# Kernel optimization log

Hardware: AMD Instinct MI355X
Metric: run time of the kernel (lower is better)

## Reference

```python
import jax, jax.numpy as jnp
import numpy as np

BN_EPS = 1e-5


def _fps(xyz, n_centers):
    """Furthest point sampling. xyz: (B,N,3) -> idx (B,n_centers) int32.
    Deterministic start at index 0 (torch version uses randint start)."""
    B, N, _ = xyz.shape
    batch_ar = jnp.arange(B)

    def step(carry, _):
        distances, farthest = carry  # (B,N), (B,)
        center = xyz[batch_ar, farthest]  # (B,3)
        d = jnp.sum((xyz - center[:, None, :]) ** 2, axis=-1)  # (B,N)
        distances = jnp.minimum(distances, d)
        new_far = jnp.argmax(distances, axis=-1)
        return (distances, new_far), farthest

    init = (jnp.full((B, N), jnp.inf, dtype=xyz.dtype),
            jnp.zeros((B,), dtype=jnp.int32))
    _, idxs = jax.lax.scan(step, init, None, length=n_centers)  # (n_centers, B)
    return idxs.T  # (B, n_centers)


def _knn_group(xyz, centers, k):
    """xyz:(B,N,3), centers:(B,M,3) -> patches (B,M,k,3) center-relative."""
    # (B,M,N) squared distances
    dists = jnp.sum((centers[:, :, None, :] - xyz[:, None, :, :]) ** 2, axis=-1)
    _, idx = jax.lax.top_k(-dists, k)  # (B,M,k) smallest distances
    # gather neighbor coords: (B,M,k,3)
    patches = jnp.take_along_axis(xyz[:, None, :, :], idx[..., None], axis=2)
    return patches - centers[:, :, None, :]


def _bn_eval(x, gamma, beta):
    # BatchNorm1d in eval mode: running_mean=0, running_var=1
    return x * (gamma / jnp.sqrt(1.0 + BN_EPS)) + beta


def _mini_pointnet(patches, W1, b1, g1, bt1, W2, b2, g2, bt2, W3, b3, g3, bt3):
    B, M, k, C = patches.shape
    x = patches.reshape(B * M * k, C)
    x = jax.nn.relu(_bn_eval(x @ W1 + b1, g1, bt1))
    x = jax.nn.relu(_bn_eval(x @ W2 + b2, g2, bt2))
    x = jax.nn.relu(_bn_eval(x @ W3 + b3, g3, bt3))
    x = x.reshape(B * M, k, -1).max(axis=1)
    return x.reshape(B, M, -1)


def setup_inputs() -> dict:
    key = jax.random.key(0)
    ks = jax.random.split(key, 8)
    B, N = 16, 16384
    embed = 256

    def lin(kk, fan_in, fan_out):
        bound = 1.0 / np.sqrt(fan_in)
        k1, k2 = jax.random.split(kk)
        W = jax.random.uniform(k1, (fan_in, fan_out), jnp.float32, -bound, bound)
        b = jax.random.uniform(k2, (fan_out,), jnp.float32, -bound, bound)
        return W, b

    W1, b1 = lin(ks[1], 3, 64)
    W2, b2 = lin(ks[2], 64, 128)
    W3, b3 = lin(ks[3], 128, embed)
    return {
        "xyz": jax.random.normal(ks[0], (B, N, 3), jnp.float32),
        "W1": W1, "b1": b1, "g1": jnp.ones((64,)), "bt1": jnp.zeros((64,)),
        "W2": W2, "b2": b2, "g2": jnp.ones((128,)), "bt2": jnp.zeros((128,)),
        "W3": W3, "b3": b3, "g3": jnp.ones((embed,)), "bt3": jnp.zeros((embed,)),
        "n_centers": 256,
        "k": 32,
    }


def reference(xyz, W1, b1, g1, bt1, W2, b2, g2, bt2, W3, b3, g3, bt3,
              n_centers, k):
    center_idx = _fps(xyz, n_centers)  # (B, M)
    centers = jnp.take_along_axis(xyz, center_idx[..., None], axis=1)  # (B,M,3)
    patches = _knn_group(xyz, centers, k)  # (B,M,k,3)
    tokens = _mini_pointnet(patches, W1, b1, g1, bt1, W2, b2, g2, bt2,
                            W3, b3, g3, bt3)
    return tokens, centers
```

## Files before the change

### kernel.cpp

```cpp
#include <hip/hip_runtime.h>

constexpr int B   = 16;
constexpr int N   = 16384;
constexpr int M   = 256;
constexpr int K   = 32;
constexpr int EMB = 256;

__device__ __forceinline__ float sqdist(float px, float py, float pz,
                                        float cx, float cy, float cz) {
  float dx = __fsub_rn(px, cx);
  float dy = __fsub_rn(py, cy);
  float dz = __fsub_rn(pz, cz);
  return __fadd_rn(__fadd_rn(__fmul_rn(dx, dx), __fmul_rn(dy, dy)),
                   __fmul_rn(dz, dz));
}

constexpr int FT = 1024;
constexpr int FW = FT / 64;

__global__ __launch_bounds__(FT) void fps_kernel(
    const float* __restrict__ xyz, float* __restrict__ centers) {
  const int b = blockIdx.x;
  const int tid = threadIdx.x;
  const int lane = tid & 63;
  const int wid = tid >> 6;
  const int l15 = lane & 15;
  const float* base = xyz + (size_t)b * N * 3;
  const float4* b4 = (const float4*)base;

  __shared__ float4 s_d[4][FT];
  __shared__ float s_pv[2][FW];
  __shared__ int s_pn[2][FW];
  __shared__ int s_flag[FW];

  const float inf = __builtin_inff();
#pragma unroll
  for (int c = 0; c < 4; ++c) s_d[c][tid] = make_float4(inf, inf, inf, inf);
  if (tid < FW) s_flag[tid] = 0;

  float cx = base[0], cy = base[1], cz = base[2];
  __syncthreads();

  const int f0 = tid * 12;

  for (int it = 0; it < M; ++it) {
    if (tid == 0) {
      float* co = centers + ((size_t)b * M + it) * 3;
      co[0] = cx; co[1] = cy; co[2] = cz;
    }
    const int p = it & 1;

    float bv = -1.0f;
    int bj = 0;

#define FPS_UPD(D, J, X, Y, Z) {                           \
    float dx = __fsub_rn((X), cx);                         \
    float dy = __fsub_rn((Y), cy);                         \
    float dz = __fsub_rn((Z), cz);                         \
    float dd = __fadd_rn(__fadd_rn(__fmul_rn(dx, dx),      \
                                   __fmul_rn(dy, dy)),     \
                         __fmul_rn(dz, dz));               \
    float nd = fminf(D, dd);                               \
    D = nd;                                                \
    bool g = nd > bv;                                      \
    bv = g ? nd : bv;                                      \
    bj = g ? (J) : bj; }

#pragma unroll
    for (int c = 0; c < 4; ++c) {
      float4 qa = b4[f0 + c * 3 + 0];
      float4 qb = b4[f0 + c * 3 + 1];
      float4 qc = b4[f0 + c * 3 + 2];
      float4 dq = s_d[c][tid];
      FPS_UPD(dq.x, c * 4 + 0, qa.x, qa.y, qa.z)
      FPS_UPD(dq.y, c * 4 + 1, qa.w, qb.x, qb.y)
      FPS_UPD(dq.z, c * 4 + 2, qb.z, qb.w, qc.x)
      FPS_UPD(dq.w, c * 4 + 3, qc.y, qc.z, qc.w)
      s_d[c][tid] = dq;
    }
#undef FPS_UPD

    int bn = (tid << 4) + bj;

#pragma unroll
    for (int mm = 32; mm >= 1; mm >>= 1) {
      float ov = __shfl_xor(bv, mm, 64);
      int on = __shfl_xor(bn, mm, 64);
      if (ov > bv || (ov == bv && on < bn)) { bv = ov; bn = on; }
    }

    if (lane == 0) {
      s_pv[p][wid] = bv;
      s_pn[p][wid] = bn;
      asm volatile("s_waitcnt lgkmcnt(0)" ::: "memory");
      s_flag[wid] = it + 1;
    }

    {
      volatile int* vf = s_flag;
      while (!__all(vf[l15] >= it + 1)) {}
    }
    asm volatile("" ::: "memory");

    float v = s_pv[p][l15];
    int n = s_pn[p][l15];
#pragma unroll
    for (int mm = 1; mm <= 8; mm <<= 1) {
      float ov = __shfl_xor(v, mm, 16);
      int on = __shfl_xor(n, mm, 16);
      if (ov > v || (ov == v && on < n)) { v = ov; n = on; }
    }
    cx = base[(size_t)n * 3 + 0];
    cy = base[(size_t)n * 3 + 1];
    cz = base[(size_t)n * 3 + 2];
  }
}

constexpr int KT = 256;
constexpr int CAP = 512;
constexpr int NBUCKET = 1024;

__global__ __launch_bounds__(KT) void knn_kernel(
    const float* __restrict__ xyz, const float* __restrict__ centers,
    float* __restrict__ patches) {
  const int blk = blockIdx.x;
  const int b = blk >> 8;
  const int tid = threadIdx.x;
  const float* base = xyz + (size_t)b * N * 3;

  __shared__ int hist[NBUCKET];
  __shared__ unsigned cb[CAP];
  __shared__ int ci[CAP];
  __shared__ int s_nin, s_ncand, s_tb;
  __shared__ int s_wsum[KT / 64];
  __shared__ float s_cc[3];

  if (tid == 0) {
    const float* c = centers + (size_t)blk * 3;
    s_cc[0] = c[0]; s_cc[1] = c[1]; s_cc[2] = c[2];
    s_nin = 0; s_ncand = 0;
  }
  for (int i = tid; i < NBUCKET; i += KT) hist[i] = 0;
  __syncthreads();

  const float cx = s_cc[0], cy = s_cc[1], cz = s_cc[2];

  for (int n = tid; n < N; n += KT) {
    float d = sqdist(base[n * 3], base[n * 3 + 1], base[n * 3 + 2], cx, cy, cz);
    atomicAdd(&hist[__float_as_uint(d) >> 21], 1);
  }
  __syncthreads();

  int h0[4];
  int loc = 0;
#pragma unroll
  for (int i = 0; i < 4; ++i) { h0[i] = hist[tid * 4 + i]; loc += h0[i]; }
  int lane = tid & 63, wid = tid >> 6;
  int scan = loc;
  for (int off = 1; off < 64; off <<= 1) {
    int o = __shfl_up(scan, off, 64);
    if (lane >= off) scan += o;
  }
  if (lane == 63) s_wsum[wid] = scan;
  __syncthreads();
  int woff = 0;
  for (int w = 0; w < wid; ++w) woff += s_wsum[w];
  int c0 = woff + scan - loc;
#pragma unroll
  for (int i = 0; i < 4; ++i) {
    int c1 = c0 + h0[i];
    if (c0 < K && c1 >= K) s_tb = tid * 4 + i;
    c0 = c1;
  }
  __syncthreads();
  const int tb = s_tb;
  const unsigned lo = (unsigned)tb << 21;
  const unsigned hi = (unsigned)(tb + 1) << 21;

  for (int n = tid; n < N; n += KT) {
    float x = base[n * 3], y = base[n * 3 + 1], z = base[n * 3 + 2];
    float d = sqdist(x, y, z, cx, cy, cz);
    unsigned bits = __float_as_uint(d);
    if (bits < lo) {
      int pos = atomicAdd(&s_nin, 1);
      float* p = patches + ((size_t)blk * K + pos) * 3;
      p[0] = __fsub_rn(x, cx); p[1] = __fsub_rn(y, cy); p[2] = __fsub_rn(z, cz);
    } else if (bits < hi) {
      int q = atomicAdd(&s_ncand, 1);
      if (q < CAP) { cb[q] = bits; ci[q] = n; }
    }
  }
  __syncthreads();

  const int nin = s_nin;
  const int ncand = min(s_ncand, CAP);
  const int nsel = K - nin;
  for (int j = tid; j < ncand; j += KT) {
    unsigned bj = cb[j];
    int ij = ci[j];
    int rank = 0;
    for (int i2 = 0; i2 < ncand; ++i2) {
      unsigned bv = cb[i2];
      int iv = ci[i2];
      rank += (bv < bj || (bv == bj && iv < ij)) ? 1 : 0;
    }
    if (rank < nsel) {
      float x = base[ij * 3], y = base[ij * 3 + 1], z = base[ij * 3 + 2];
      float* p = patches + ((size_t)blk * K + nin + rank) * 3;
      p[0] = __fsub_rn(x, cx); p[1] = __fsub_rn(y, cy); p[2] = __fsub_rn(z, cz);
    }
  }
}

constexpr int MT = 128;

__global__ __launch_bounds__(MT) void mlp_kernel(
    const float* __restrict__ patches,
    const float* __restrict__ W1, const float* __restrict__ b1,
    const float* __restrict__ g1, const float* __restrict__ bt1,
    const float* __restrict__ W2, const float* __restrict__ b2,
    const float* __restrict__ g2, const float* __restrict__ bt2,
    const float* __restrict__ W3, const float* __restrict__ b3,
    const float* __restrict__ g3, const float* __restrict__ bt3,
    float* __restrict__ tokens) {
  const int pm = blockIdx.x;
  const int tid = threadIdx.x;
  __shared__ float xs[3][K];
  __shared__ float h1s[64 * K];
  __shared__ float h2s[128 * K];
  __shared__ float pms[2][EMB];

  const float* patch = patches + (size_t)pm * (K * 3);
  if (tid < 96) xs[tid % 3][tid / 3] = patch[tid];
  __syncthreads();

  const int cg = tid & 63;
  const int half = tid >> 6;
  const int pt0 = half * 16;
  const float rs = 1.0f / sqrtf(1.0f + 1e-5f);

  {
    const int c = cg;
    const float w0 = W1[c], w1 = W1[64 + c], w2 = W1[128 + c];
    const float bb = b1[c];
    const float sc = g1[c] * rs, be = bt1[c];
    float o[16];
#pragma unroll
    for (int p = 0; p < 16; ++p) {
      int pt = pt0 + p;
      float a = xs[0][pt] * w0 + xs[1][pt] * w1 + xs[2][pt] * w2 + bb;
      o[p] = fmaxf(a * sc + be, 0.0f);
    }
    const int so = (c & 7) << 2;
#pragma unroll
    for (int p4 = 0; p4 < 16; p4 += 4) {
      *(float4*)&h1s[c * K + ((pt0 + p4) ^ so)] =
          make_float4(o[p4], o[p4 + 1], o[p4 + 2], o[p4 + 3]);
    }
  }
  __syncthreads();

  {
    const int c = cg * 2;
    float acc0[16], acc1[16];
    const float bb0 = b2[c], bb1 = b2[c + 1];
#pragma unroll
    for (int p = 0; p < 16; ++p) { acc0[p] = bb0; acc1[p] = bb1; }
    for (int k = 0; k < 64; ++k) {
      const float2 w = *(const float2*)(W2 + k * 128 + c);
      const int so = (k & 7) << 2;
      float4 x0 = *(const float4*)&h1s[k * K + ((pt0 + 0) ^ so)];
      float4 x1 = *(const float4*)&h1s[k * K + ((pt0 + 4) ^ so)];
      float4 x2 = *(const float4*)&h1s[k * K + ((pt0 + 8) ^ so)];
      float4 x3 = *(const float4*)&h1s[k * K + ((pt0 + 12) ^ so)];
      float xv[16] = {x0.x, x0.y, x0.z, x0.w, x1.x, x1.y, x1.z, x1.w,
                      x2.x, x2.y, x2.z, x2.w, x3.x, x3.y, x3.z, x3.w};
#pragma unroll
      for (int p = 0; p < 16; ++p) {
        acc0[p] += xv[p] * w.x;
        acc1[p] += xv[p] * w.y;
      }
    }
    const float sc0 = g2[c] * rs, be0 = bt2[c];
    const float sc1 = g2[c + 1] * rs, be1 = bt2[c + 1];
    float o0[16], o1[16];
#pragma unroll
    for (int p = 0; p < 16; ++p) {
      o0[p] = fmaxf(acc0[p] * sc0 + be0, 0.0f);
      o1[p] = fmaxf(acc1[p] * sc1 + be1, 0.0f);
    }
    const int soa = (c & 7) << 2, sob = ((c + 1) & 7) << 2;
#pragma unroll
    for (int p4 = 0; p4 < 16; p4 += 4) {
      *(float4*)&h2s[c * K + ((pt0 + p4) ^ soa)] =
          make_float4(o0[p4], o0[p4 + 1], o0[p4 + 2], o0[p4 + 3]);
      *(float4*)&h2s[(c + 1) * K + ((pt0 + p4) ^ sob)] =
          make_float4(o1[p4], o1[p4 + 1], o1[p4 + 2], o1[p4 + 3]);
    }
  }
  __syncthreads();

  {
    const int c = cg * 4;
    float acc[4][16];
#pragma unroll
    for (int i = 0; i < 4; ++i) {
      const float bb = b3[c + i];
#pragma unroll
      for (int p = 0; p < 16; ++p) acc[i][p] = bb;
    }
    for (int k = 0; k < 128; ++k) {
      const float4 w = *(const float4*)(W3 + (size_t)k * 256 + c);
      const int so = (k & 7) << 2;
      float4 x0 = *(const float4*)&h2s[k * K + ((pt0 + 0) ^ so)];
      float4 x1 = *(const float4*)&h2s[k * K + ((pt0 + 4) ^ so)];
      float4 x2 = *(const float4*)&h2s[k * K + ((pt0 + 8) ^ so)];
      float4 x3 = *(const float4*)&h2s[k * K + ((pt0 + 12) ^ so)];
      float xv[16] = {x0.x, x0.y, x0.z, x0.w, x1.x, x1.y, x1.z, x1.w,
                      x2.x, x2.y, x2.z, x2.w, x3.x, x3.y, x3.z, x3.w};
#pragma unroll
      for (int p = 0; p < 16; ++p) {
        acc[0][p] += xv[p] * w.x;
        acc[1][p] += xv[p] * w.y;
        acc[2][p] += xv[p] * w.z;
        acc[3][p] += xv[p] * w.w;
      }
    }
#pragma unroll
    for (int i = 0; i < 4; ++i) {
      const float sc = g3[c + i] * rs, be = bt3[c + i];
      float mx = 0.0f;
#pragma unroll
      for (int p = 0; p < 16; ++p)
        mx = fmaxf(mx, fmaxf(acc[i][p] * sc + be, 0.0f));
      pms[half][c + i] = mx;
    }
  }
  __syncthreads();

  {
    const int c2 = tid * 2;
    float* to = tokens + (size_t)pm * EMB;
    to[c2] = fmaxf(pms[0][c2], pms[1][c2]);
    to[c2 + 1] = fmaxf(pms[0][c2 + 1], pms[1][c2 + 1]);
  }
}

extern "C" void kernel_launch(void* const* d_in, const int* in_sizes, int n_in,
                              void* d_out, int out_size, void* d_ws,
                              size_t ws_size, hipStream_t stream) {
  const float* xyz = (const float*)d_in[0];
  const float* W1 = (const float*)d_in[1];
  const float* b1 = (const float*)d_in[2];
  const float* g1 = (const float*)d_in[3];
  const float* bt1 = (const float*)d_in[4];
  const float* W2 = (const float*)d_in[5];
  const float* b2 = (const float*)d_in[6];
  const float* g2 = (const float*)d_in[7];
  const float* bt2 = (const float*)d_in[8];
  const float* W3 = (const float*)d_in[9];
  const float* b3 = (const float*)d_in[10];
  const float* g3 = (const float*)d_in[11];
  const float* bt3 = (const float*)d_in[12];

  float* tokens = (float*)d_out;
  float* centers = tokens + (size_t)B * M * EMB;
  float* patches = (float*)d_ws;

  fps_kernel<<<B, FT, 0, stream>>>(xyz, centers);
  knn_kernel<<<B * M, KT, 0, stream>>>(xyz, centers, patches);
  mlp_kernel<<<B * M, MT, 0, stream>>>(patches, W1, b1, g1, bt1, W2, b2, g2,
                                       bt2, W3, b3, g3, bt3, tokens);
}
```

Baseline: 835.7 us.

## Keep FPS points and distances resident in AGPRs instead of reloading each iteration

The FPS kernel now loads each thread's 16 points once before the iteration loop and keeps them, together with the running min-distances, in registers. Inline asm constraints pin these 64 values to accumulation registers so they survive the 1024-thread launch bound. This removes the per-iteration global reloads of xyz and the LDS round trip for the distance array. It also adds an s_sleep inside the cross-wave spin-wait to ease LDS polling pressure, at the risk of extra wake-up latency on the serial 256-step critical path.

```diff
diff --git a/kernel.cpp b/kernel.cpp
--- a/kernel.cpp
+++ b/kernel.cpp
@@ -17,6 +17,9 @@
 
 constexpr int FT = 1024;
 constexpr int FW = FT / 64;
+
+#define FPS_REP16(X) X(0) X(1) X(2) X(3) X(4) X(5) X(6) X(7) X(8) X(9) \
+  X(10) X(11) X(12) X(13) X(14) X(15)
 
 __global__ __launch_bounds__(FT) void fps_kernel(
     const float* __restrict__ xyz, float* __restrict__ centers) {
@@ -28,22 +31,52 @@
   const float* base = xyz + (size_t)b * N * 3;
   const float4* b4 = (const float4*)base;
 
-  __shared__ float4 s_d[4][FT];
   __shared__ float s_pv[2][FW];
   __shared__ int s_pn[2][FW];
   __shared__ int s_flag[FW];
 
+#define FPS_DECL(i) float px##i, py##i, pz##i, ds##i;
+  FPS_REP16(FPS_DECL)
+#undef FPS_DECL
+
+  const int f0 = tid * 12;
+#define FPS_LD4(c, A, Bp, C, D) {                          \
+    float4 qa = b4[f0 + (c) * 3 + 0];                      \
+    float4 qb = b4[f0 + (c) * 3 + 1];                      \
+    float4 qc = b4[f0 + (c) * 3 + 2];                      \
+    px##A = qa.x;  py##A = qa.y;  pz##A = qa.z;            \
+    px##Bp = qa.w; py##Bp = qb.x; pz##Bp = qb.y;           \
+    px##C = qb.z;  py##C = qb.w;  pz##C = qc.x;            \
+    px##D = qc.y;  py##D = qc.z;  pz##D = qc.w; }
+  FPS_LD4(0, 0, 1, 2, 3)
+  FPS_LD4(1, 4, 5, 6, 7)
+  FPS_LD4(2, 8, 9, 10, 11)
+  FPS_LD4(3, 12, 13, 14, 15)
+#undef FPS_LD4
   const float inf = __builtin_inff();
-#pragma unroll
-  for (int c = 0; c < 4; ++c) s_d[c][tid] = make_float4(inf, inf, inf, inf);
+#define FPS_DINIT(i) ds##i = inf;
+  FPS_REP16(FPS_DINIT)
+#undef FPS_DINIT
+
   if (tid < FW) s_flag[tid] = 0;
 
   float cx = base[0], cy = base[1], cz = base[2];
   __syncthreads();
 
-  const int f0 = tid * 12;
+#define PIN8(a0, a1, a2, a3, a4, a5, a6, a7)               \
+  asm volatile("" : "+a"(a0), "+a"(a1), "+a"(a2), "+a"(a3),\
+                    "+a"(a4), "+a"(a5), "+a"(a6), "+a"(a7));
 
   for (int it = 0; it < M; ++it) {
+    PIN8(px0, py0, pz0, px1, py1, pz1, px2, py2)
+    PIN8(pz2, px3, py3, pz3, px4, py4, pz4, px5)
+    PIN8(py5, pz5, px6, py6, pz6, px7, py7, pz7)
+    PIN8(px8, py8, pz8, px9, py9, pz9, px10, py10)
+    PIN8(pz10, px11, py11, pz11, px12, py12, pz12, px13)
+    PIN8(py13, pz13, px14, py14, pz14, px15, py15, pz15)
+    PIN8(ds0, ds1, ds2, ds3, ds4, ds5, ds6, ds7)
+    PIN8(ds8, ds9, ds10, ds11, ds12, ds13, ds14, ds15)
+
     if (tid == 0) {
       float* co = centers + ((size_t)b * M + it) * 3;
       co[0] = cx; co[1] = cy; co[2] = cz;
@@ -53,31 +86,19 @@
     float bv = -1.0f;
     int bj = 0;
 
-#define FPS_UPD(D, J, X, Y, Z) {                           \
-    float dx = __fsub_rn((X), cx);                         \
-    float dy = __fsub_rn((Y), cy);                         \
-    float dz = __fsub_rn((Z), cz);                         \
+#define FPS_UPD(i) {                                       \
+    float dx = __fsub_rn(px##i, cx);                       \
+    float dy = __fsub_rn(py##i, cy);                       \
+    float dz = __fsub_rn(pz##i, cz);                       \
     float dd = __fadd_rn(__fadd_rn(__fmul_rn(dx, dx),      \
                                    __fmul_rn(dy, dy)),     \
                          __fmul_rn(dz, dz));               \
-    float nd = fminf(D, dd);                               \
-    D = nd;                                                \
+    float nd = fminf(ds##i, dd);                           \
+    ds##i = nd;                                            \
     bool g = nd > bv;                                      \
     bv = g ? nd : bv;                                      \
-    bj = g ? (J) : bj; }
-
-#pragma unroll
-    for (int c = 0; c < 4; ++c) {
-      float4 qa = b4[f0 + c * 3 + 0];
-      float4 qb = b4[f0 + c * 3 + 1];
-      float4 qc = b4[f0 + c * 3 + 2];
-      float4 dq = s_d[c][tid];
-      FPS_UPD(dq.x, c * 4 + 0, qa.x, qa.y, qa.z)
-      FPS_UPD(dq.y, c * 4 + 1, qa.w, qb.x, qb.y)
-      FPS_UPD(dq.z, c * 4 + 2, qb.z, qb.w, qc.x)
-      FPS_UPD(dq.w, c * 4 + 3, qc.y, qc.z, qc.w)
-      s_d[c][tid] = dq;
-    }
+    bj = g ? (i) : bj; }
+    FPS_REP16(FPS_UPD)
 #undef FPS_UPD
 
     int bn = (tid << 4) + bj;
@@ -98,7 +119,7 @@
 
     {
       volatile int* vf = s_flag;
-      while (!__all(vf[l15] >= it + 1)) {}
+      while (!__all(vf[l15] >= it + 1)) { __builtin_amdgcn_s_sleep(1); }
     }
     asm volatile("" ::: "memory");
 
@@ -114,6 +135,7 @@
     cy = base[(size_t)n * 3 + 1];
     cz = base[(size_t)n * 3 + 2];
   }
+#undef PIN8
 }
 
 constexpr int KT = 256;
```

Result: slower. 960.9 us (+15.0%).
